# Performance work log

Measured on AMD Instinct MI355X. Metric: run time of the kernel, lower is better.

Reference implementation:

```python
import jax, jax.numpy as jnp
import numpy as np
from jax import lax


def _sobel3d_kernels():
    # Standard separable 3D Sobel: derivative d=[-1,0,1] along one axis,
    # smoothing s=[1,2,1] along the other two. Axes order (D, H, W).
    d = np.array([-1.0, 0.0, 1.0], dtype=np.float32)
    s = np.array([1.0, 2.0, 1.0], dtype=np.float32)
    kx = np.einsum('i,j,k->ijk', d, s, s)  # derivative along D
    ky = np.einsum('i,j,k->ijk', s, d, s)  # derivative along H
    kz = np.einsum('i,j,k->ijk', s, s, d)  # derivative along W
    # Stack as [Cout=3, Cin=1, 3, 3, 3] -> one conv computes x,y,z grads at once.
    return jnp.asarray(np.stack([kx, ky, kz])[:, None])


_DN = ('NCDHW', 'OIDHW', 'NCDHW')


def _conv3(x, k):
    # x: [N, 1, D, H, W], k: [3, 1, 3, 3, 3] -> [N, 3, D-2, H-2, W-2]
    # torch F.conv3d and lax conv are both cross-correlation; VALID padding.
    return lax.conv_general_dilated(x, k, (1, 1, 1), 'VALID', dimension_numbers=_DN)


def _g2(inp, k):
    # inp: [B, D, H, W, C] (channels last, as the torch module permutes)
    b, dd, hh, ww, c = inp.shape
    x = jnp.transpose(inp, (0, 4, 1, 2, 3)).reshape(b * c, 1, dd, hh, ww)
    g1 = _conv3(x, k)                                  # [B*C, 3, D-2, H-2, W-2]
    mag = jnp.sqrt(jnp.sum(g1 * g1, axis=1, keepdims=True))  # first-order magnitude
    g2 = _conv3(mag, k)                                # [B*C, 3, D-4, H-4, W-4]
    gx, gy, gz = g2[:, 0], g2[:, 1], g2[:, 2]
    # Faithful to source: sqrt(x^2 + y^2) + z^2 (note: z is squared, not inside sqrt)
    out = jnp.sqrt(gx * gx + gy * gy) + gz * gz        # [B*C, D-4, H-4, W-4]
    return out.reshape(b, c, *out.shape[1:])


def setup_inputs() -> dict:
    key = jax.random.key(0)
    k1, k2 = jax.random.split(key)
    pred = jax.random.normal(k1, (2, 64, 64, 64, 32), dtype=jnp.float32)
    hr = jax.random.normal(k2, (2, 64, 64, 64, 32), dtype=jnp.float32)
    return {'pred': pred, 'hr': hr}


def reference(pred, hr):
    k = _sobel3d_kernels()
    return jnp.mean(jnp.abs(_g2(pred, k) - _g2(hr, k)))
```

## Files before the change

kernel.cpp:

```cpp
#include <hip/hip_runtime.h>
#include <hip/hip_fp16.h>


constexpr int BDIM = 256;
constexpr size_t IN_B = 8388608;
constexpr int IN_D = 131072;
constexpr int IN_H = 2048;
constexpr int M = 62;
constexpr int F = 60;
constexpr int C = 32;
constexpr int MROW = M * C;
constexpr size_t MAGSZ = (size_t)M * M * MROW;
constexpr size_t PLANE = (size_t)M * MROW;

__device__ __forceinline__ float2 ld2(const float* p) {
    return *reinterpret_cast<const float2*>(p);
}

struct Raw1 { float2 v[12]; };
struct P1W  { float2 A[2], B[2], Cc[2]; };

__device__ __forceinline__ void p1_issue(const float* __restrict__ pbase,
                                         int zplane, int y0, int lo, Raw1& r)
{
#pragma unroll
    for (int j = 0; j < 4; ++j) {
        const float* rowp = pbase + (size_t)zplane * IN_D + (size_t)(y0 + j) * IN_H;
        r.v[j * 3 + 0] = ld2(rowp + lo);
        r.v[j * 3 + 1] = ld2(rowp + lo + C);
        r.v[j * 3 + 2] = ld2(rowp + lo + 2 * C);
    }
}

__device__ __forceinline__ void p1_reduce(const Raw1& r, P1W& W)
{
    float2 SX[4], DX[4];
#pragma unroll
    for (int j = 0; j < 4; ++j) {
        float2 a = r.v[j * 3], b = r.v[j * 3 + 1], c = r.v[j * 3 + 2];
        SX[j] = make_float2(a.x + 2.f * b.x + c.x, a.y + 2.f * b.y + c.y);
        DX[j] = make_float2(c.x - a.x, c.y - a.y);
    }
#pragma unroll
    for (int k = 0; k < 2; ++k) {
        W.A[k]  = make_float2(SX[k].x + 2.f * SX[k+1].x + SX[k+2].x,
                              SX[k].y + 2.f * SX[k+1].y + SX[k+2].y);
        W.B[k]  = make_float2(SX[k+2].x - SX[k].x, SX[k+2].y - SX[k].y);
        W.Cc[k] = make_float2(DX[k].x + 2.f * DX[k+1].x + DX[k+2].x,
                              DX[k].y + 2.f * DX[k+1].y + DX[k+2].y);
    }
}

__device__ __forceinline__ void p1_emit(const P1W& W0, const P1W& W1, const P1W& W2,
                                        __half* __restrict__ mag, int z, int y0,
                                        int lo, bool xok)
{
    if (!xok) return;
#pragma unroll
    for (int k = 0; k < 2; ++k) {
        float gxx = W2.A[k].x - W0.A[k].x;
        float gxy = W2.A[k].y - W0.A[k].y;
        float gyx = W0.B[k].x + 2.f * W1.B[k].x + W2.B[k].x;
        float gyy = W0.B[k].y + 2.f * W1.B[k].y + W2.B[k].y;
        float gzx = W0.Cc[k].x + 2.f * W1.Cc[k].x + W2.Cc[k].x;
        float gzy = W0.Cc[k].y + 2.f * W1.Cc[k].y + W2.Cc[k].y;
        float mx = sqrtf(gxx * gxx + gyx * gyx + gzx * gzx);
        float my = sqrtf(gxy * gxy + gyy * gyy + gzy * gzy);
        *reinterpret_cast<__half2*>(mag + ((size_t)z * M + (y0 + k)) * MROW + lo)
            = __floats2half2_rn(mx, my);
    }
}

__global__ __launch_bounds__(BDIM) void sobel_mag_stream(
    const float* __restrict__ pred, const float* __restrict__ hr,
    __half* __restrict__ magbase, int bstart)
{
    const int xt = blockIdx.x & 3, yt = blockIdx.x >> 2;
    const int zc = blockIdx.y;
    const int gz = blockIdx.z;
    const int b  = bstart + (gz >> 1);
    const float* __restrict__ in  = (gz & 1) ? hr : pred;
    __half*      __restrict__ mag = magbase + (size_t)gz * MAGSZ;

    const int y0 = yt * 2;
    const int z0 = zc * 8;
    const int zn = min(8, M - z0);
    const int xraw = xt * 16 + (threadIdx.x >> 4);
    const bool xok = xraw < M;
    const int x = min(xraw, M - 1);
    const int lo = x * C + ((threadIdx.x & 15) << 1);

    const float* pbase = in + (size_t)b * IN_B;

    Raw1 r;
    P1W W0, W1, W2;
    p1_issue(pbase, z0 + 0, y0, lo, r); p1_reduce(r, W0);
    p1_issue(pbase, z0 + 1, y0, lo, r); p1_reduce(r, W1);
    p1_issue(pbase, z0 + 2, y0, lo, r); p1_reduce(r, W2);
    int z = 0;
    for (;;) {
        bool more = (z + 1 < zn);
        if (more) p1_issue(pbase, z0 + z + 3, y0, lo, r);
        p1_emit(W0, W1, W2, mag, z0 + z, y0, lo, xok);
        if (!more) break;
        ++z;
        p1_reduce(r, W0);
        more = (z + 1 < zn);
        if (more) p1_issue(pbase, z0 + z + 3, y0, lo, r);
        p1_emit(W1, W2, W0, mag, z0 + z, y0, lo, xok);
        if (!more) break;
        ++z;
        p1_reduce(r, W1);
        more = (z + 1 < zn);
        if (more) p1_issue(pbase, z0 + z + 3, y0, lo, r);
        p1_emit(W2, W0, W1, mag, z0 + z, y0, lo, xok);
        if (!more) break;
        ++z;
        p1_reduce(r, W2);
    }
}

struct Raw2 { __half2 v[12]; };
struct P2W  { float2 A[2], B[2], Cc[2]; };

__device__ __forceinline__ void p2_issue(const __half* __restrict__ mbase,
                                         int zplane, int y0, int lo, Raw2& r)
{
#pragma unroll
    for (int j = 0; j < 4; ++j) {
        const __half* rowp = mbase + (size_t)zplane * PLANE + (size_t)(y0 + j) * MROW;
        r.v[j * 3 + 0] = *reinterpret_cast<const __half2*>(rowp + lo);
        r.v[j * 3 + 1] = *reinterpret_cast<const __half2*>(rowp + lo + C);
        r.v[j * 3 + 2] = *reinterpret_cast<const __half2*>(rowp + lo + 2 * C);
    }
}

__device__ __forceinline__ void p2_reduce(const Raw2& r, P2W& W)
{
    float2 SX[4], DX[4];
#pragma unroll
    for (int j = 0; j < 4; ++j) {
        float2 a = __half22float2(r.v[j * 3]);
        float2 b = __half22float2(r.v[j * 3 + 1]);
        float2 c = __half22float2(r.v[j * 3 + 2]);
        SX[j] = make_float2(a.x + 2.f * b.x + c.x, a.y + 2.f * b.y + c.y);
        DX[j] = make_float2(c.x - a.x, c.y - a.y);
    }
#pragma unroll
    for (int k = 0; k < 2; ++k) {
        W.A[k]  = make_float2(SX[k].x + 2.f * SX[k+1].x + SX[k+2].x,
                              SX[k].y + 2.f * SX[k+1].y + SX[k+2].y);
        W.B[k]  = make_float2(SX[k+2].x - SX[k].x, SX[k+2].y - SX[k].y);
        W.Cc[k] = make_float2(DX[k].x + 2.f * DX[k+1].x + DX[k+2].x,
                              DX[k].y + 2.f * DX[k+1].y + DX[k+2].y);
    }
}

__device__ __forceinline__ void p2_emit(const P2W& P0, const P2W& P1, const P2W& P2,
                                        const P2W& H0, const P2W& H1, const P2W& H2,
                                        float& acc)
{
#pragma unroll
    for (int k = 0; k < 2; ++k) {
        float gxPx = P2.A[k].x - P0.A[k].x;
        float gxPy = P2.A[k].y - P0.A[k].y;
        float gyPx = P0.B[k].x + 2.f * P1.B[k].x + P2.B[k].x;
        float gyPy = P0.B[k].y + 2.f * P1.B[k].y + P2.B[k].y;
        float gzPx = P0.Cc[k].x + 2.f * P1.Cc[k].x + P2.Cc[k].x;
        float gzPy = P0.Cc[k].y + 2.f * P1.Cc[k].y + P2.Cc[k].y;
        float gxHx = H2.A[k].x - H0.A[k].x;
        float gxHy = H2.A[k].y - H0.A[k].y;
        float gyHx = H0.B[k].x + 2.f * H1.B[k].x + H2.B[k].x;
        float gyHy = H0.B[k].y + 2.f * H1.B[k].y + H2.B[k].y;
        float gzHx = H0.Cc[k].x + 2.f * H1.Cc[k].x + H2.Cc[k].x;
        float gzHy = H0.Cc[k].y + 2.f * H1.Cc[k].y + H2.Cc[k].y;
        float oPx = sqrtf(gxPx * gxPx + gyPx * gyPx) + gzPx * gzPx;
        float oPy = sqrtf(gxPy * gxPy + gyPy * gyPy) + gzPy * gzPy;
        float oHx = sqrtf(gxHx * gxHx + gyHx * gyHx) + gzHx * gzHx;
        float oHy = sqrtf(gxHy * gxHy + gyHy * gyHy) + gzHy * gzHy;
        acc += fabsf(oPx - oHx) + fabsf(oPy - oHy);
    }
}

__global__ __launch_bounds__(BDIM) void sobel2_stream(
    const __half* __restrict__ magbase, float* __restrict__ partial, int bstart)
{
    const int xt = blockIdx.x & 3, yt = blockIdx.x >> 2;
    const int zc = blockIdx.y;
    const int b  = bstart + blockIdx.z;
    const __half* __restrict__ magP = magbase + (size_t)(2 * blockIdx.z) * MAGSZ;
    const __half* __restrict__ magH = magP + MAGSZ;

    const int y0 = yt * 2;
    const int z0 = zc * 6;
    const int zn = 6;
    const int xraw = xt * 16 + (threadIdx.x >> 4);
    const bool xok = xraw < F;
    const int x = min(xraw, F - 1);
    const int lo = x * C + ((threadIdx.x & 15) << 1);

    Raw2 rp, rh;
    P2W P0, P1, P2, H0, H1, H2;
    p2_issue(magP, z0 + 0, y0, lo, rp); p2_issue(magH, z0 + 0, y0, lo, rh);
    p2_reduce(rp, P0); p2_reduce(rh, H0);
    p2_issue(magP, z0 + 1, y0, lo, rp); p2_issue(magH, z0 + 1, y0, lo, rh);
    p2_reduce(rp, P1); p2_reduce(rh, H1);
    p2_issue(magP, z0 + 2, y0, lo, rp); p2_issue(magH, z0 + 2, y0, lo, rh);
    p2_reduce(rp, P2); p2_reduce(rh, H2);

    float acc = 0.f;
    int z = 0;
    for (;;) {
        bool more = (z + 1 < zn);
        if (more) { p2_issue(magP, z0 + z + 3, y0, lo, rp);
                    p2_issue(magH, z0 + z + 3, y0, lo, rh); }
        if (xok) p2_emit(P0, P1, P2, H0, H1, H2, acc);
        if (!more) break;
        ++z;
        p2_reduce(rp, P0); p2_reduce(rh, H0);
        more = (z + 1 < zn);
        if (more) { p2_issue(magP, z0 + z + 3, y0, lo, rp);
                    p2_issue(magH, z0 + z + 3, y0, lo, rh); }
        if (xok) p2_emit(P1, P2, P0, H1, H2, H0, acc);
        if (!more) break;
        ++z;
        p2_reduce(rp, P1); p2_reduce(rh, H1);
        more = (z + 1 < zn);
        if (more) { p2_issue(magP, z0 + z + 3, y0, lo, rp);
                    p2_issue(magH, z0 + z + 3, y0, lo, rh); }
        if (xok) p2_emit(P2, P0, P1, H2, H0, H1, acc);
        if (!more) break;
        ++z;
        p2_reduce(rp, P2); p2_reduce(rh, H2);
    }

    for (int o = 32; o > 0; o >>= 1) acc += __shfl_down(acc, o, 64);
    __shared__ float sred[BDIM / 64];
    const int lane = threadIdx.x & 63, wv = threadIdx.x >> 6;
    if (lane == 0) sred[wv] = acc;
    __syncthreads();
    if (threadIdx.x == 0) {
        float t = 0.f;
#pragma unroll
        for (int i = 0; i < BDIM / 64; ++i) t += sred[i];
        partial[(size_t)b * 1200 + (size_t)zc * 120 + blockIdx.x] = t;
    }
}

__global__ __launch_bounds__(BDIM) void finalize_kernel(
    const float* __restrict__ partial, float* __restrict__ out)
{
    double a = 0.0;
    for (int i = threadIdx.x; i < 2400; i += BDIM) a += (double)partial[i];
    for (int o = 32; o > 0; o >>= 1) a += __shfl_down(a, o, 64);
    __shared__ double sd[BDIM / 64];
    const int lane = threadIdx.x & 63, wv = threadIdx.x >> 6;
    if (lane == 0) sd[wv] = a;
    __syncthreads();
    if (threadIdx.x == 0) {
        double t = 0.0;
#pragma unroll
        for (int i = 0; i < BDIM / 64; ++i) t += sd[i];
        out[0] = (float)(t / 13824000.0);
    }
}

extern "C" void kernel_launch(void* const* d_in, const int* in_sizes, int n_in,
                              void* d_out, int out_size, void* d_ws, size_t ws_size,
                              hipStream_t stream)
{
    const float* pred = (const float*)d_in[0];
    const float* hr   = (const float*)d_in[1];

    float* partial = (float*)d_ws;
    __half* magbase = (__half*)((char*)d_ws + 65536);

    const bool merged = ws_size >= (size_t)65536 + 4 * MAGSZ * sizeof(__half);
    if (merged) {
        sobel_mag_stream<<<dim3(124, 8, 4), BDIM, 0, stream>>>(pred, hr, magbase, 0);
        sobel2_stream<<<dim3(120, 10, 2), BDIM, 0, stream>>>(magbase, partial, 0);
    } else {
        for (int b = 0; b < 2; ++b) {
            sobel_mag_stream<<<dim3(124, 8, 2), BDIM, 0, stream>>>(pred, hr, magbase, b);
            sobel2_stream<<<dim3(120, 10, 1), BDIM, 0, stream>>>(magbase, partial, b);
        }
    }
    finalize_kernel<<<1, BDIM, 0, stream>>>(partial, (float*)d_out);
}
```

Baseline: 253.1 us.

## Widen both Sobel passes to four channels per thread with 128-bit loads

```diff
diff --git a/kernel.cpp b/kernel.cpp
--- a/kernel.cpp
+++ b/kernel.cpp
@@ -13,12 +13,26 @@
 constexpr size_t MAGSZ = (size_t)M * M * MROW;
 constexpr size_t PLANE = (size_t)M * MROW;
 
-__device__ __forceinline__ float2 ld2(const float* p) {
-    return *reinterpret_cast<const float2*>(p);
-}
-
-struct Raw1 { float2 v[12]; };
-struct P1W  { float2 A[2], B[2], Cc[2]; };
+union H2U { __half2 h; unsigned u; };
+
+__device__ __forceinline__ float4 ld4(const float* p) {
+    return *reinterpret_cast<const float4*>(p);
+}
+__device__ __forceinline__ float4 sm3(float4 a, float4 b, float4 c) {
+    return make_float4(a.x + 2.f * b.x + c.x, a.y + 2.f * b.y + c.y,
+                       a.z + 2.f * b.z + c.z, a.w + 2.f * b.w + c.w);
+}
+__device__ __forceinline__ float4 df2(float4 a, float4 c) {
+    return make_float4(c.x - a.x, c.y - a.y, c.z - a.z, c.w - a.w);
+}
+__device__ __forceinline__ float4 h4tof4(uint2 u) {
+    H2U a, b; a.u = u.x; b.u = u.y;
+    float2 l = __half22float2(a.h), h = __half22float2(b.h);
+    return make_float4(l.x, l.y, h.x, h.y);
+}
+
+struct Raw1 { float4 v[12]; };
+struct P1W  { float4 A[2], B[2], Cc[2]; };
 
 __device__ __forceinline__ void p1_issue(const float* __restrict__ pbase,
                                          int zplane, int y0, int lo, Raw1& r)
@@ -26,56 +40,51 @@
 #pragma unroll
     for (int j = 0; j < 4; ++j) {
         const float* rowp = pbase + (size_t)zplane * IN_D + (size_t)(y0 + j) * IN_H;
-        r.v[j * 3 + 0] = ld2(rowp + lo);
-        r.v[j * 3 + 1] = ld2(rowp + lo + C);
-        r.v[j * 3 + 2] = ld2(rowp + lo + 2 * C);
+        r.v[j * 3 + 0] = ld4(rowp + lo);
+        r.v[j * 3 + 1] = ld4(rowp + lo + C);
+        r.v[j * 3 + 2] = ld4(rowp + lo + 2 * C);
     }
 }
 
 __device__ __forceinline__ void p1_reduce(const Raw1& r, P1W& W)
 {
-    float2 SX[4], DX[4];
+    float4 SX[4], DX[4];
 #pragma unroll
     for (int j = 0; j < 4; ++j) {
-        float2 a = r.v[j * 3], b = r.v[j * 3 + 1], c = r.v[j * 3 + 2];
-        SX[j] = make_float2(a.x + 2.f * b.x + c.x, a.y + 2.f * b.y + c.y);
-        DX[j] = make_float2(c.x - a.x, c.y - a.y);
+        SX[j] = sm3(r.v[j * 3], r.v[j * 3 + 1], r.v[j * 3 + 2]);
+        DX[j] = df2(r.v[j * 3], r.v[j * 3 + 2]);
     }
 #pragma unroll
     for (int k = 0; k < 2; ++k) {
-        W.A[k]  = make_float2(SX[k].x + 2.f * SX[k+1].x + SX[k+2].x,
-                              SX[k].y + 2.f * SX[k+1].y + SX[k+2].y);
-        W.B[k]  = make_float2(SX[k+2].x - SX[k].x, SX[k+2].y - SX[k].y);
-        W.Cc[k] = make_float2(DX[k].x + 2.f * DX[k+1].x + DX[k+2].x,
-                              DX[k].y + 2.f * DX[k+1].y + DX[k+2].y);
+        W.A[k]  = sm3(SX[k], SX[k + 1], SX[k + 2]);
+        W.B[k]  = df2(SX[k], SX[k + 2]);
+        W.Cc[k] = sm3(DX[k], DX[k + 1], DX[k + 2]);
     }
 }
 
 __device__ __forceinline__ void p1_emit(const P1W& W0, const P1W& W1, const P1W& W2,
-                                        __half* __restrict__ mag, int z, int y0,
-                                        int lo, bool xok)
-{
-    if (!xok) return;
+                                        __half* __restrict__ mag, int z, int y0, int lo)
+{
 #pragma unroll
     for (int k = 0; k < 2; ++k) {
-        float gxx = W2.A[k].x - W0.A[k].x;
-        float gxy = W2.A[k].y - W0.A[k].y;
-        float gyx = W0.B[k].x + 2.f * W1.B[k].x + W2.B[k].x;
-        float gyy = W0.B[k].y + 2.f * W1.B[k].y + W2.B[k].y;
-        float gzx = W0.Cc[k].x + 2.f * W1.Cc[k].x + W2.Cc[k].x;
-        float gzy = W0.Cc[k].y + 2.f * W1.Cc[k].y + W2.Cc[k].y;
-        float mx = sqrtf(gxx * gxx + gyx * gyx + gzx * gzx);
-        float my = sqrtf(gxy * gxy + gyy * gyy + gzy * gzy);
-        *reinterpret_cast<__half2*>(mag + ((size_t)z * M + (y0 + k)) * MROW + lo)
-            = __floats2half2_rn(mx, my);
-    }
-}
-
-__global__ __launch_bounds__(BDIM) void sobel_mag_stream(
+        float4 gx = df2(W0.A[k], W2.A[k]);
+        float4 gy = sm3(W0.B[k], W1.B[k], W2.B[k]);
+        float4 gz = sm3(W0.Cc[k], W1.Cc[k], W2.Cc[k]);
+        float4 m = make_float4(sqrtf(gx.x * gx.x + gy.x * gy.x + gz.x * gz.x),
+                               sqrtf(gx.y * gx.y + gy.y * gy.y + gz.y * gz.y),
+                               sqrtf(gx.z * gx.z + gy.z * gy.z + gz.z * gz.z),
+                               sqrtf(gx.w * gx.w + gy.w * gy.w + gz.w * gz.w));
+        H2U o0, o1; o0.h = __floats2half2_rn(m.x, m.y); o1.h = __floats2half2_rn(m.z, m.w);
+        *reinterpret_cast<uint2*>(mag + ((size_t)z * M + (y0 + k)) * MROW + lo)
+            = make_uint2(o0.u, o1.u);
+    }
+}
+
+__global__ __launch_bounds__(BDIM, 3) void sobel_mag_stream(
     const float* __restrict__ pred, const float* __restrict__ hr,
     __half* __restrict__ magbase, int bstart)
 {
-    const int xt = blockIdx.x & 3, yt = blockIdx.x >> 2;
+    const int xt = blockIdx.x & 1, yt = blockIdx.x >> 1;
     const int zc = blockIdx.y;
     const int gz = blockIdx.z;
     const int b  = bstart + (gz >> 1);
@@ -85,10 +94,8 @@
     const int y0 = yt * 2;
     const int z0 = zc * 8;
     const int zn = min(8, M - z0);
-    const int xraw = xt * 16 + (threadIdx.x >> 4);
-    const bool xok = xraw < M;
-    const int x = min(xraw, M - 1);
-    const int lo = x * C + ((threadIdx.x & 15) << 1);
+    const int x  = xt * 30 + (threadIdx.x >> 3);
+    const int lo = x * C + ((threadIdx.x & 7) << 2);
 
     const float* pbase = in + (size_t)b * IN_B;
 
@@ -101,103 +108,93 @@
     for (;;) {
         bool more = (z + 1 < zn);
         if (more) p1_issue(pbase, z0 + z + 3, y0, lo, r);
-        p1_emit(W0, W1, W2, mag, z0 + z, y0, lo, xok);
+        p1_emit(W0, W1, W2, mag, z0 + z, y0, lo);
         if (!more) break;
         ++z;
         p1_reduce(r, W0);
         more = (z + 1 < zn);
         if (more) p1_issue(pbase, z0 + z + 3, y0, lo, r);
-        p1_emit(W1, W2, W0, mag, z0 + z, y0, lo, xok);
+        p1_emit(W1, W2, W0, mag, z0 + z, y0, lo);
         if (!more) break;
         ++z;
         p1_reduce(r, W1);
         more = (z + 1 < zn);
         if (more) p1_issue(pbase, z0 + z + 3, y0, lo, r);
-        p1_emit(W2, W0, W1, mag, z0 + z, y0, lo, xok);
+        p1_emit(W2, W0, W1, mag, z0 + z, y0, lo);
         if (!more) break;
         ++z;
         p1_reduce(r, W2);
     }
 }
 
-struct Raw2 { __half2 v[12]; };
-struct P2W  { float2 A[2], B[2], Cc[2]; };
+struct Raw2 { uint2 v[9]; };
+struct P2W  { float4 A, B, Cc; };
 
 __device__ __forceinline__ void p2_issue(const __half* __restrict__ mbase,
                                          int zplane, int y0, int lo, Raw2& r)
 {
 #pragma unroll
-    for (int j = 0; j < 4; ++j) {
+    for (int j = 0; j < 3; ++j) {
         const __half* rowp = mbase + (size_t)zplane * PLANE + (size_t)(y0 + j) * MROW;
-        r.v[j * 3 + 0] = *reinterpret_cast<const __half2*>(rowp + lo);
-        r.v[j * 3 + 1] = *reinterpret_cast<const __half2*>(rowp + lo + C);
-        r.v[j * 3 + 2] = *reinterpret_cast<const __half2*>(rowp + lo + 2 * C);
+        r.v[j * 3 + 0] = *reinterpret_cast<const uint2*>(rowp + lo);
+        r.v[j * 3 + 1] = *reinterpret_cast<const uint2*>(rowp + lo + C);
+        r.v[j * 3 + 2] = *reinterpret_cast<const uint2*>(rowp + lo + 2 * C);
     }
 }
 
 __device__ __forceinline__ void p2_reduce(const Raw2& r, P2W& W)
 {
-    float2 SX[4], DX[4];
-#pragma unroll
-    for (int j = 0; j < 4; ++j) {
-        float2 a = __half22float2(r.v[j * 3]);
-        float2 b = __half22float2(r.v[j * 3 + 1]);
-        float2 c = __half22float2(r.v[j * 3 + 2]);
-        SX[j] = make_float2(a.x + 2.f * b.x + c.x, a.y + 2.f * b.y + c.y);
-        DX[j] = make_float2(c.x - a.x, c.y - a.y);
-    }
-#pragma unroll
-    for (int k = 0; k < 2; ++k) {
-        W.A[k]  = make_float2(SX[k].x + 2.f * SX[k+1].x + SX[k+2].x,
-                              SX[k].y + 2.f * SX[k+1].y + SX[k+2].y);
-        W.B[k]  = make_float2(SX[k+2].x - SX[k].x, SX[k+2].y - SX[k].y);
-        W.Cc[k] = make_float2(DX[k].x + 2.f * DX[k+1].x + DX[k+2].x,
-                              DX[k].y + 2.f * DX[k+1].y + DX[k+2].y);
-    }
+    float4 SX[3], DX[3];
+#pragma unroll
+    for (int j = 0; j < 3; ++j) {
+        float4 a = h4tof4(r.v[j * 3]);
+        float4 b = h4tof4(r.v[j * 3 + 1]);
+        float4 c = h4tof4(r.v[j * 3 + 2]);
+        SX[j] = sm3(a, b, c);
+        DX[j] = df2(a, c);
+    }
+    W.A  = sm3(SX[0], SX[1], SX[2]);
+    W.B  = df2(SX[0], SX[2]);
+    W.Cc = sm3(DX[0], DX[1], DX[2]);
 }
 
 __device__ __forceinline__ void p2_emit(const P2W& P0, const P2W& P1, const P2W& P2,
                                         const P2W& H0, const P2W& H1, const P2W& H2,
                                         float& acc)
 {
-#pragma unroll
-    for (int k = 0; k < 2; ++k) {
-        float gxPx = P2.A[k].x - P0.A[k].x;
-        float gxPy = P2.A[k].y - P0.A[k].y;
-        float gyPx = P0.B[k].x + 2.f * P1.B[k].x + P2.B[k].x;
-        float gyPy = P0.B[k].y + 2.f * P1.B[k].y + P2.B[k].y;
-        float gzPx = P0.Cc[k].x + 2.f * P1.Cc[k].x + P2.Cc[k].x;
-        float gzPy = P0.Cc[k].y + 2.f * P1.Cc[k].y + P2.Cc[k].y;
-        float gxHx = H2.A[k].x - H0.A[k].x;
-        float gxHy = H2.A[k].y - H0.A[k].y;
-        float gyHx = H0.B[k].x + 2.f * H1.B[k].x + H2.B[k].x;
-        float gyHy = H0.B[k].y + 2.f * H1.B[k].y + H2.B[k].y;
-        float gzHx = H0.Cc[k].x + 2.f * H1.Cc[k].x + H2.Cc[k].x;
-        float gzHy = H0.Cc[k].y + 2.f * H1.Cc[k].y + H2.Cc[k].y;
-        float oPx = sqrtf(gxPx * gxPx + gyPx * gyPx) + gzPx * gzPx;
-        float oPy = sqrtf(gxPy * gxPy + gyPy * gyPy) + gzPy * gzPy;
-        float oHx = sqrtf(gxHx * gxHx + gyHx * gyHx) + gzHx * gzHx;
-        float oHy = sqrtf(gxHy * gxHy + gyHy * gyHy) + gzHy * gzHy;
-        acc += fabsf(oPx - oHx) + fabsf(oPy - oHy);
-    }
-}
-
-__global__ __launch_bounds__(BDIM) void sobel2_stream(
+    float4 gxP = df2(P0.A, P2.A);
+    float4 gyP = sm3(P0.B, P1.B, P2.B);
+    float4 gzP = sm3(P0.Cc, P1.Cc, P2.Cc);
+    float4 gxH = df2(H0.A, H2.A);
+    float4 gyH = sm3(H0.B, H1.B, H2.B);
+    float4 gzH = sm3(H0.Cc, H1.Cc, H2.Cc);
+    acc += fabsf((sqrtf(gxP.x * gxP.x + gyP.x * gyP.x) + gzP.x * gzP.x)
+               - (sqrtf(gxH.x * gxH.x + gyH.x * gyH.x) + gzH.x * gzH.x));
+    acc += fabsf((sqrtf(gxP.y * gxP.y + gyP.y * gyP.y) + gzP.y * gzP.y)
+               - (sqrtf(gxH.y * gxH.y + gyH.y * gyH.y) + gzH.y * gzH.y));
+    acc += fabsf((sqrtf(gxP.z * gxP.z + gyP.z * gyP.z) + gzP.z * gzP.z)
+               - (sqrtf(gxH.z * gxH.z + gyH.z * gyH.z) + gzH.z * gzH.z));
+    acc += fabsf((sqrtf(gxP.w * gxP.w + gyP.w * gyP.w) + gzP.w * gzP.w)
+               - (sqrtf(gxH.w * gxH.w + gyH.w * gyH.w) + gzH.w * gzH.w));
+}
+
+__global__ __launch_bounds__(BDIM, 3) void sobel2_stream(
     const __half* __restrict__ magbase, float* __restrict__ partial, int bstart)
 {
-    const int xt = blockIdx.x & 3, yt = blockIdx.x >> 2;
+    const int xt = blockIdx.x & 1, yt = blockIdx.x >> 1;
     const int zc = blockIdx.y;
     const int b  = bstart + blockIdx.z;
     const __half* __restrict__ magP = magbase + (size_t)(2 * blockIdx.z) * MAGSZ;
     const __half* __restrict__ magH = magP + MAGSZ;
 
-    const int y0 = yt * 2;
+    const int y0 = yt;
     const int z0 = zc * 6;
     const int zn = 6;
-    const int xraw = xt * 16 + (threadIdx.x >> 4);
-    const bool xok = xraw < F;
-    const int x = min(xraw, F - 1);
-    const int lo = x * C + ((threadIdx.x & 15) << 1);
+    const int xi = threadIdx.x >> 3;
+    const int xraw = xt * 30 + xi;
+    const bool xok = xi < 30;
+    const int xload = min(xraw, F - 1);
+    const int lo = xload * C + ((threadIdx.x & 7) << 2);
 
     Raw2 rp, rh;
     P2W P0, P1, P2, H0, H1, H2;
@@ -277,11 +274,11 @@
 
     const bool merged = ws_size >= (size_t)65536 + 4 * MAGSZ * sizeof(__half);
     if (merged) {
-        sobel_mag_stream<<<dim3(124, 8, 4), BDIM, 0, stream>>>(pred, hr, magbase, 0);
+        sobel_mag_stream<<<dim3(62, 8, 4), BDIM, 0, stream>>>(pred, hr, magbase, 0);
         sobel2_stream<<<dim3(120, 10, 2), BDIM, 0, stream>>>(magbase, partial, 0);
     } else {
         for (int b = 0; b < 2; ++b) {
-            sobel_mag_stream<<<dim3(124, 8, 2), BDIM, 0, stream>>>(pred, hr, magbase, b);
+            sobel_mag_stream<<<dim3(62, 8, 2), BDIM, 0, stream>>>(pred, hr, magbase, b);
             sobel2_stream<<<dim3(120, 10, 1), BDIM, 0, stream>>>(magbase, partial, b);
         }
     }
```

New measurement: 400.3 us. +58.2%, slower.
